# Kernel tuning notes

Hardware: AMD Instinct MI355X
Metric: run time of the kernel (lower is better)

## Reference

```python
import jax, jax.numpy as jnp
import numpy as np

B, S, E, H = 2, 2048, 1024, 16
Dh = E // H  # 64
KEEP = 0.9   # 1 - dropout_p
INV_SCALE = 1.0  # forward() default; call site does not pass inv_scale


def setup_inputs() -> dict:
    key = jax.random.key(0)
    ks = jax.random.split(key, 12)
    query = jax.random.normal(ks[0], (B, S, E), dtype=jnp.float32)
    key_t = jax.random.normal(ks[1], (B, S, E), dtype=jnp.float32)
    value = jax.random.normal(ks[2], (B, S, E), dtype=jnp.float32)
    attn_mask = jax.random.randint(ks[3], (B, S), 0, 2, dtype=jnp.int32)
    # pre-scaled inverted dropout keep-mask (deterministic stand-in for F.dropout)
    dropout_mask = (jax.random.uniform(ks[4], (B, H, S, S)) < KEEP).astype(jnp.float32) / KEEP
    Wq = jax.random.normal(ks[5], (E, E), dtype=jnp.float32) * 0.02
    bq = jnp.zeros((E,), dtype=jnp.float32)
    Wk = jax.random.normal(ks[6], (E, E), dtype=jnp.float32) * 0.02
    bk = jnp.zeros((E,), dtype=jnp.float32)
    Wv = jax.random.normal(ks[7], (E, E), dtype=jnp.float32) * 0.02
    bv = jnp.zeros((E,), dtype=jnp.float32)
    return {"query": query, "key": key_t, "value": value, "attn_mask": attn_mask,
            "dropout_mask": dropout_mask, "Wq": Wq, "bq": bq, "Wk": Wk, "bk": bk,
            "Wv": Wv, "bv": bv}


def _heads(x, W, b):
    # Linear then split heads: (B,S,E) -> (B,H,S,Dh)
    y = x @ W.T + b
    return y.reshape(B, S, H, Dh).transpose(0, 2, 1, 3)


def reference(query, key, value, attn_mask, dropout_mask, Wq, bq, Wk, bk, Wv, bv):
    q = _heads(query, Wq, bq)
    k = _heads(key, Wk, bk)
    v = _heads(value, Wv, bv)
    scores = jnp.einsum("bhqd,bhkd->bhqk", q, k) / INV_SCALE
    pad = (attn_mask == 0)[:, None, None, :]  # (B,1,1,S) True = masked
    scores = jnp.where(pad, -jnp.inf, scores)
    attn = jax.nn.softmax(scores, axis=-1) * dropout_mask
    out = jnp.einsum("bhqk,bhkd->bhqd", attn, v)  # (B,H,S,Dh)
    return out
```

## Files before the change

### kernel.cpp

```cpp
#include <hip/hip_runtime.h>

#define B_ 2
#define S_ 2048
#define E_ 1024
#define H_ 16
#define DH 64
#define MM (B_*S_)
#define BHN (B_*H_)

typedef unsigned short u16;
typedef unsigned int u32;
typedef __attribute__((ext_vector_type(8))) __bf16 bf16x8;
typedef __attribute__((ext_vector_type(4))) float f32x4;
typedef __attribute__((ext_vector_type(8))) u16 u16x8;
typedef __attribute__((ext_vector_type(4))) u16 u16x4;

static __device__ __forceinline__ u16 f2bf(float f) {
  u32 u = __builtin_bit_cast(u32, f);
  u += 0x7fffu + ((u >> 16) & 1u);
  return (u16)(u >> 16);
}
static __device__ __forceinline__ float bf2f(u16 h) {
  return __builtin_bit_cast(float, (u32)h << 16);
}
static __device__ __forceinline__ u32 sw(u32 byte) {
  return byte ^ (((byte >> 7) & 7u) << 4);
}
static __device__ __forceinline__ bf16x8 frag(const u16* lds, u32 byte) {
  return *(const bf16x8*)((const char*)lds + byte);
}
static __device__ __forceinline__ f32x4 mfma16(bf16x8 a, bf16x8 b, f32x4 c) {
  return __builtin_amdgcn_mfma_f32_16x16x32_bf16(a, b, c, 0, 0, 0);
}
static __device__ __forceinline__ void gload_lds16(const u16* g, u16* lds_base) {
  __builtin_amdgcn_global_load_lds(
      (const __attribute__((address_space(1))) u32*)g,
      (__attribute__((address_space(3))) u32*)lds_base, 16, 0, 0);
}

#define L2E 1.44269504088896340736f

struct SplitArg { const float* s; u16* h; u16* l; int n4; };

__global__ void split6_kernel(SplitArg a0, SplitArg a1, SplitArg a2,
                              SplitArg a3, SplitArg a4, SplitArg a5) {
  SplitArg A = (blockIdx.z == 0) ? a0 : (blockIdx.z == 1) ? a1 : (blockIdx.z == 2) ? a2
             : (blockIdx.z == 3) ? a3 : (blockIdx.z == 4) ? a4 : a5;
  int i = blockIdx.x * blockDim.x + threadIdx.x;
  int stride = gridDim.x * blockDim.x;
  if (A.l) {
    for (; i < A.n4; i += stride) {
      float4 v = ((const float4*)A.s)[i];
      u16x4 h, l;
      h.x = f2bf(v.x); l.x = f2bf(v.x - bf2f(h.x));
      h.y = f2bf(v.y); l.y = f2bf(v.y - bf2f(h.y));
      h.z = f2bf(v.z); l.z = f2bf(v.z - bf2f(h.z));
      h.w = f2bf(v.w); l.w = f2bf(v.w - bf2f(h.w));
      ((u16x4*)A.h)[i] = h;
      ((u16x4*)A.l)[i] = l;
    }
  } else {
    for (; i < A.n4; i += stride) {
      float4 v = ((const float4*)A.s)[i];
      u16x4 h;
      h.x = f2bf(v.x); h.y = f2bf(v.y); h.z = f2bf(v.z); h.w = f2bf(v.w);
      ((u16x4*)A.h)[i] = h;
    }
  }
}

__global__ void pack_mask(const int* __restrict__ am, u32* __restrict__ pm) {
  int w = threadIdx.x;
  if (w < 128) {
    int base = (w >> 6) * 2048 + (w & 63) * 32;
    u32 bits = 0;
#pragma unroll
    for (int j = 0; j < 8; ++j) {
      int4 v = *(const int4*)(am + base + j * 4);
      bits |= (v.x ? 1u : 0u) << (4 * j) | (v.y ? 1u : 0u) << (4 * j + 1) |
              (v.z ? 1u : 0u) << (4 * j + 2) | (v.w ? 1u : 0u) << (4 * j + 3);
    }
    pm[w] = bits;
  }
}

struct ProjArgs {
  const u16* xhi; const u16* xlo; const u16* whi; const u16* wlo;
  const float* bias; u16* ohi; u16* olo; int mode;
};

__global__ __launch_bounds__(256, 3) void proj_gemm(ProjArgs a0, ProjArgs a1, ProjArgs a2) {
  ProjArgs A = (blockIdx.z == 0) ? a0 : (blockIdx.z == 1) ? a1 : a2;
  __shared__ u16 As[128 * 64];
  __shared__ u16 Bs[128 * 64];
  const int t = threadIdx.x;
  const int l = t & 63, wid = t >> 6;
  const int g = l >> 4, ln = l & 15;
  const int wm = wid >> 1, wn = wid & 1;
  int bid = blockIdx.y * 8 + blockIdx.x;
  int sid = (bid & 7) * 32 + (bid >> 3);
  const int m0 = (sid >> 3) * 128, e0 = (sid & 7) * 128;

  f32x4 acc[4][4] = {};
  const int nkt = (A.mode == 2) ? 32 : 48;

  for (int kt = 0; kt < nkt; ++kt) {
    int kp = kt * 64;
    const u16* asrc = (kp < 2048) ? A.xhi : A.xlo;
    const u16* bsrc = (kp < 1024 || kp >= 2048) ? A.whi : A.wlo;
    int kc = kp & 1023;
#pragma unroll
    for (int r = 0; r < 4; ++r) {
      int cr = wid * 4 + r;
      int row = cr * 8 + (l >> 3);
      int col = (l & 7) * 8;
      gload_lds16(asrc + (size_t)(m0 + row) * 1024 + kc + col, As + cr * 512);
      gload_lds16(bsrc + (size_t)(e0 + row) * 1024 + kc + col, Bs + cr * 512);
    }
    __syncthreads();
#pragma unroll
    for (int ks = 0; ks < 2; ++ks) {
      bf16x8 af[4], bfv[4];
#pragma unroll
      for (int i = 0; i < 4; ++i) {
        af[i] = frag(As, (u32)(wm * 64 + i * 16 + ln) * 128 + ks * 64 + g * 16);
        bfv[i] = frag(Bs, (u32)(wn * 64 + i * 16 + ln) * 128 + ks * 64 + g * 16);
      }
#pragma unroll
      for (int i = 0; i < 4; ++i)
#pragma unroll
        for (int j = 0; j < 4; ++j)
          acc[i][j] = mfma16(af[i], bfv[j], acc[i][j]);
    }
    __syncthreads();
  }

#pragma unroll
  for (int i = 0; i < 4; ++i) {
#pragma unroll
    for (int j = 0; j < 4; ++j) {
      int e = e0 + wn * 64 + j * 16 + ln;
      int h = e >> 6, d = e & 63;
      float bias = A.bias[e];
      if (A.mode < 2) {
#pragma unroll
        for (int r = 0; r < 4; ++r) {
          int m = m0 + wm * 64 + i * 16 + g * 4 + r;
          float v = acc[i][j][r] + bias;
          if (A.mode == 0) v *= L2E;
          int b = m >> 11, s = m & 2047;
          size_t idx = ((size_t)((b * 16 + h) * 2048 + s)) * 64 + d;
          u16 hv = f2bf(v);
          A.ohi[idx] = hv;
          A.olo[idx] = f2bf(v - bf2f(hv));
        }
      } else {
        int m = m0 + wm * 64 + i * 16 + g * 4;
        int b = m >> 11, s = m & 2047;
        u16x4 pv;
#pragma unroll
        for (int r = 0; r < 4; ++r) pv[r] = f2bf(acc[i][j][r] + bias);
        size_t idx = ((size_t)((b * 16 + h) * 64 + d)) * 2048 + s;
        *(u16x4*)(A.ohi + idx) = pv;
      }
    }
  }
}

__global__ __launch_bounds__(256, 2) void attn_kernel(
    const u16* __restrict__ qhi, const u16* __restrict__ qlo,
    const u16* __restrict__ khi, const u16* __restrict__ klo,
    const u16* __restrict__ vt, const u32* __restrict__ pm,
    const float* __restrict__ dmask, float* __restrict__ out) {
  __shared__ u16 Ksh[2][64 * 64];
  __shared__ u16 Ksl[2][64 * 64];
  __shared__ u16 Vs[2][64 * 64];
  __shared__ u16 Ps[4 * 16 * 64];

  const int t = threadIdx.x, l = t & 63, wid = t >> 6;
  const int g = l >> 4, ln = l & 15;

  int bid = blockIdx.y * 32 + blockIdx.x;
  int sid = (bid & 7) * 128 + (bid >> 3);
  const int qt = sid & 31, bh = sid >> 5, b = bh >> 4;
  const int q0 = qt * 64;
  const int qrow = q0 + wid * 16 + ln;
  const size_t qg = ((size_t)bh * 2048 + qrow) * 64;
  const u32* pmb = pm + b * 64;

  bf16x8 qh[2], ql[2];
#pragma unroll
  for (int ks = 0; ks < 2; ++ks) {
    qh[ks] = *(const bf16x8*)(qhi + qg + ks * 32 + g * 8);
    ql[ks] = *(const bf16x8*)(qlo + qg + ks * 32 + g * 8);
  }

  const size_t dmrow = ((size_t)bh * 2048 + qrow) * 2048;
  float4 dmc[4], dmn[4];
  auto load_dm = [&](int kt, float4* d) {
    const int k0 = kt * 64;
#pragma unroll
    for (int i = 0; i < 4; ++i)
      d[i] = *(const float4*)(dmask + dmrow + k0 + i * 16 + 4 * g);
  };

  auto stage = [&](int buf, int kt) {
    const int k0 = kt * 64;
    const size_t kbase = ((size_t)bh * 2048 + k0) * 64;
    u16* khd = Ksh[buf];
    u16* kld = Ksl[buf];
    u16* vd = Vs[buf];
#pragma unroll
    for (int r = 0; r < 2; ++r) {
      int cbase = wid * 64 + 256 * r;
      int c = cbase + l;
      int c2 = c ^ ((c >> 3) & 7);
      gload_lds16(khi + kbase + c2 * 8, khd + cbase * 8);
      gload_lds16(klo + kbase + c2 * 8, kld + cbase * 8);
      gload_lds16(vt + ((size_t)bh * 64 + (c2 >> 3)) * 2048 + k0 + (c2 & 7) * 8,
                  vd + cbase * 8);
    }
  };

  load_dm(0, dmc);
  stage(0, 0);
  __syncthreads();

  f32x4 O[4] = {};
  float Zacc = 0.f;
  const u32 psbase = (u32)(wid * 2048 + ln * 128);

#pragma unroll 2
  for (int kt = 0; kt < 32; ++kt) {
    const int buf = kt & 1;
    if (kt < 31) {
      stage(buf ^ 1, kt + 1);
      load_dm(kt + 1, dmn);
    }
    u32 m0 = pmb[2 * kt], m1 = pmb[2 * kt + 1];

    f32x4 sc[4] = {};
#pragma unroll
    for (int ks = 0; ks < 2; ++ks) {
#pragma unroll
      for (int i = 0; i < 4; ++i) {
        u32 byt = sw((u32)((i * 16 + ln) * 128 + ks * 64 + g * 16));
        bf16x8 akh = frag(Ksh[buf], byt);
        bf16x8 akl = frag(Ksl[buf], byt);
        sc[i] = mfma16(akh, qh[ks], sc[i]);
        sc[i] = mfma16(akh, ql[ks], sc[i]);
        sc[i] = mfma16(akl, qh[ks], sc[i]);
      }
    }

#pragma unroll
    for (int i = 0; i < 4; ++i) {
      u32 mm = (i < 2 ? m0 : m1) >> (((i & 1) << 4) + 4 * g);
      float e0 = (mm & 1u) ? exp2f(sc[i][0]) : 0.f;
      float e1 = (mm & 2u) ? exp2f(sc[i][1]) : 0.f;
      float e2 = (mm & 4u) ? exp2f(sc[i][2]) : 0.f;
      float e3 = (mm & 8u) ? exp2f(sc[i][3]) : 0.f;
      Zacc += (e0 + e1) + (e2 + e3);
      u16x4 p;
      p.x = f2bf(e0 * dmc[i].x);
      p.y = f2bf(e1 * dmc[i].y);
      p.z = f2bf(e2 * dmc[i].z);
      p.w = f2bf(e3 * dmc[i].w);
      *(u16x4*)((char*)Ps + sw(psbase + i * 32 + g * 8)) = p;
    }

#pragma unroll
    for (int ks = 0; ks < 2; ++ks) {
      bf16x8 bP = frag(Ps, sw(psbase + ks * 64 + g * 16));
#pragma unroll
      for (int id = 0; id < 4; ++id) {
        bf16x8 aV = frag(Vs[buf], sw((u32)((id * 16 + ln) * 128 + ks * 64 + g * 16)));
        O[id] = mfma16(aV, bP, O[id]);
      }
    }

    __syncthreads();
    if (kt < 31) {
#pragma unroll
      for (int i = 0; i < 4; ++i) dmc[i] = dmn[i];
    }
  }

  float z = Zacc;
  z += __shfl_xor(z, 16, 64);
  z += __shfl_xor(z, 32, 64);
  float rz = 1.f / z;

#pragma unroll
  for (int id = 0; id < 4; ++id) {
    float4 o;
    o.x = O[id][0] * rz; o.y = O[id][1] * rz;
    o.z = O[id][2] * rz; o.w = O[id][3] * rz;
    *(float4*)(out + qg + id * 16 + 4 * g) = o;
  }
}

extern "C" void kernel_launch(void* const* d_in, const int* in_sizes, int n_in,
                              void* d_out, int out_size, void* d_ws, size_t ws_size,
                              hipStream_t stream) {
  const float* query = (const float*)d_in[0];
  const float* keyt  = (const float*)d_in[1];
  const float* value = (const float*)d_in[2];
  const int*   amask = (const int*)d_in[3];
  const float* dmask = (const float*)d_in[4];
  const float* Wq = (const float*)d_in[5];
  const float* bq = (const float*)d_in[6];
  const float* Wk = (const float*)d_in[7];
  const float* bk = (const float*)d_in[8];
  const float* Wv = (const float*)d_in[9];
  const float* bv = (const float*)d_in[10];

  char* ws = (char*)d_ws;
  size_t off = 0;
  auto alloc = [&](size_t bytes) {
    char* p = ws + off;
    off += (bytes + 255) & ~(size_t)255;
    return p;
  };
  const size_t XB = (size_t)MM * E_ * sizeof(u16);
  const size_t WB = (size_t)E_ * E_ * sizeof(u16);

  u16 *xh[3], *xl[3], *wh[3], *wl[3];
  for (int i = 0; i < 3; ++i) { xh[i] = (u16*)alloc(XB); xl[i] = (u16*)alloc(XB); }
  for (int i = 0; i < 3; ++i) { wh[i] = (u16*)alloc(WB); wl[i] = (u16*)alloc(WB); }
  u16* q_hi = (u16*)alloc(XB);
  u16* q_lo = (u16*)alloc(XB);
  u16* k_hi = (u16*)alloc(XB);
  u16* k_lo = (u16*)alloc(XB);
  u16* v_t  = (u16*)alloc(XB);
  u32* pmask = (u32*)alloc(512);
  if (off > ws_size) return;

  SplitArg sa[6] = {
      {query, xh[0], xl[0], MM * E_ / 4}, {keyt, xh[1], xl[1], MM * E_ / 4},
      {value, xh[2], nullptr, MM * E_ / 4}, {Wq, wh[0], wl[0], E_ * E_ / 4},
      {Wk, wh[1], wl[1], E_ * E_ / 4},    {Wv, wh[2], wl[2], E_ * E_ / 4},
  };
  split6_kernel<<<dim3(512, 1, 6), 256, 0, stream>>>(sa[0], sa[1], sa[2], sa[3], sa[4], sa[5]);
  pack_mask<<<1, 128, 0, stream>>>(amask, pmask);

  ProjArgs pa[3] = {
      {xh[0], xl[0], wh[0], wl[0], bq, q_hi, q_lo, 0},
      {xh[1], xl[1], wh[1], wl[1], bk, k_hi, k_lo, 1},
      {xh[2], nullptr, wh[2], wl[2], bv, v_t, nullptr, 2},
  };
  proj_gemm<<<dim3(8, 32, 3), 256, 0, stream>>>(pa[0], pa[1], pa[2]);

  attn_kernel<<<dim3(32, 32), 256, 0, stream>>>(
      q_hi, q_lo, k_hi, k_lo, v_t, pmask, dmask, (float*)d_out);
}
```

Measured before the change: 287.2 us.

## Process 128 query rows per attention block to reuse K/V tiles across two sub-tiles

Each wave now handles two 16-row query sub-tiles, so a block covers 128 query rows and the grid shrinks to 512 blocks. Every K/V tile staged in shared memory is reused for twice as many MFMAs, halving K/V global traffic per output. The dropout-mask prefetch into registers one iteration ahead is replaced by in-loop loads, and the unroll pragma is dropped. This raises register pressure and leaves fewer blocks to fill the CUs, and the dropout-mask stream, which dominates memory traffic, is unchanged.

New measurement: 327.5 us. +14.0%, slower.

```diff
diff --git a/kernel.cpp b/kernel.cpp
--- a/kernel.cpp
+++ b/kernel.cpp
@@ -175,34 +175,33 @@
   __shared__ u16 Ksh[2][64 * 64];
   __shared__ u16 Ksl[2][64 * 64];
   __shared__ u16 Vs[2][64 * 64];
-  __shared__ u16 Ps[4 * 16 * 64];
+  __shared__ u16 Ps[4 * 32 * 64];
 
   const int t = threadIdx.x, l = t & 63, wid = t >> 6;
   const int g = l >> 4, ln = l & 15;
 
-  int bid = blockIdx.y * 32 + blockIdx.x;
-  int sid = (bid & 7) * 128 + (bid >> 3);
-  const int qt = sid & 31, bh = sid >> 5, b = bh >> 4;
-  const int q0 = qt * 64;
-  const int qrow = q0 + wid * 16 + ln;
-  const size_t qg = ((size_t)bh * 2048 + qrow) * 64;
+  int bid = blockIdx.x;
+  int sid = (bid & 7) * 64 + (bid >> 3);
+  const int qt = sid & 15, bh = sid >> 4, b = bh >> 4;
+  const int q0 = qt * 128;
   const u32* pmb = pm + b * 64;
 
-  bf16x8 qh[2], ql[2];
-#pragma unroll
-  for (int ks = 0; ks < 2; ++ks) {
-    qh[ks] = *(const bf16x8*)(qhi + qg + ks * 32 + g * 8);
-    ql[ks] = *(const bf16x8*)(qlo + qg + ks * 32 + g * 8);
-  }
-
-  const size_t dmrow = ((size_t)bh * 2048 + qrow) * 2048;
-  float4 dmc[4], dmn[4];
-  auto load_dm = [&](int kt, float4* d) {
-    const int k0 = kt * 64;
-#pragma unroll
-    for (int i = 0; i < 4; ++i)
-      d[i] = *(const float4*)(dmask + dmrow + k0 + i * 16 + 4 * g);
-  };
+  size_t qg[2]; size_t dmrow[2];
+#pragma unroll
+  for (int qs = 0; qs < 2; ++qs) {
+    int qrow = q0 + wid * 32 + qs * 16 + ln;
+    qg[qs] = ((size_t)bh * 2048 + qrow) * 64;
+    dmrow[qs] = ((size_t)bh * 2048 + qrow) * 2048;
+  }
+
+  bf16x8 qh[2][2], ql[2][2];
+#pragma unroll
+  for (int qs = 0; qs < 2; ++qs)
+#pragma unroll
+    for (int ks = 0; ks < 2; ++ks) {
+      qh[qs][ks] = *(const bf16x8*)(qhi + qg[qs] + ks * 32 + g * 8);
+      ql[qs][ks] = *(const bf16x8*)(qlo + qg[qs] + ks * 32 + g * 8);
+    }
 
   auto stage = [&](int buf, int kt) {
     const int k0 = kt * 64;
@@ -222,24 +221,26 @@
     }
   };
 
-  load_dm(0, dmc);
   stage(0, 0);
   __syncthreads();
 
-  f32x4 O[4] = {};
-  float Zacc = 0.f;
-  const u32 psbase = (u32)(wid * 2048 + ln * 128);
-
-#pragma unroll 2
+  f32x4 O[2][4] = {};
+  float Zacc[2] = {0.f, 0.f};
+  const u32 psb = (u32)(wid * 4096);
+
   for (int kt = 0; kt < 32; ++kt) {
     const int buf = kt & 1;
-    if (kt < 31) {
-      stage(buf ^ 1, kt + 1);
-      load_dm(kt + 1, dmn);
-    }
+    const int k0 = kt * 64;
+    if (kt < 31) stage(buf ^ 1, kt + 1);
+    float4 dm[2][4];
+#pragma unroll
+    for (int qs = 0; qs < 2; ++qs)
+#pragma unroll
+      for (int i = 0; i < 4; ++i)
+        dm[qs][i] = *(const float4*)(dmask + dmrow[qs] + k0 + i * 16 + 4 * g);
     u32 m0 = pmb[2 * kt], m1 = pmb[2 * kt + 1];
 
-    f32x4 sc[4] = {};
+    f32x4 sc[2][4] = {};
 #pragma unroll
     for (int ks = 0; ks < 2; ++ks) {
 #pragma unroll
@@ -247,56 +248,61 @@
         u32 byt = sw((u32)((i * 16 + ln) * 128 + ks * 64 + g * 16));
         bf16x8 akh = frag(Ksh[buf], byt);
         bf16x8 akl = frag(Ksl[buf], byt);
-        sc[i] = mfma16(akh, qh[ks], sc[i]);
-        sc[i] = mfma16(akh, ql[ks], sc[i]);
-        sc[i] = mfma16(akl, qh[ks], sc[i]);
-      }
-    }
-
-#pragma unroll
-    for (int i = 0; i < 4; ++i) {
-      u32 mm = (i < 2 ? m0 : m1) >> (((i & 1) << 4) + 4 * g);
-      float e0 = (mm & 1u) ? exp2f(sc[i][0]) : 0.f;
-      float e1 = (mm & 2u) ? exp2f(sc[i][1]) : 0.f;
-      float e2 = (mm & 4u) ? exp2f(sc[i][2]) : 0.f;
-      float e3 = (mm & 8u) ? exp2f(sc[i][3]) : 0.f;
-      Zacc += (e0 + e1) + (e2 + e3);
-      u16x4 p;
-      p.x = f2bf(e0 * dmc[i].x);
-      p.y = f2bf(e1 * dmc[i].y);
-      p.z = f2bf(e2 * dmc[i].z);
-      p.w = f2bf(e3 * dmc[i].w);
-      *(u16x4*)((char*)Ps + sw(psbase + i * 32 + g * 8)) = p;
-    }
+#pragma unroll
+        for (int qs = 0; qs < 2; ++qs) {
+          sc[qs][i] = mfma16(akh, qh[qs][ks], sc[qs][i]);
+          sc[qs][i] = mfma16(akh, ql[qs][ks], sc[qs][i]);
+          sc[qs][i] = mfma16(akl, qh[qs][ks], sc[qs][i]);
+        }
+      }
+    }
+
+#pragma unroll
+    for (int qs = 0; qs < 2; ++qs)
+#pragma unroll
+      for (int i = 0; i < 4; ++i) {
+        u32 mm = (i < 2 ? m0 : m1) >> (((i & 1) << 4) + 4 * g);
+        float e0 = (mm & 1u) ? exp2f(sc[qs][i][0]) : 0.f;
+        float e1 = (mm & 2u) ? exp2f(sc[qs][i][1]) : 0.f;
+        float e2 = (mm & 4u) ? exp2f(sc[qs][i][2]) : 0.f;
+        float e3 = (mm & 8u) ? exp2f(sc[qs][i][3]) : 0.f;
+        Zacc[qs] += (e0 + e1) + (e2 + e3);
+        u16x4 p;
+        p.x = f2bf(e0 * dm[qs][i].x);
+        p.y = f2bf(e1 * dm[qs][i].y);
+        p.z = f2bf(e2 * dm[qs][i].z);
+        p.w = f2bf(e3 * dm[qs][i].w);
+        *(u16x4*)((char*)Ps + sw(psb + (qs * 16 + ln) * 128 + i * 32 + g * 8)) = p;
+      }
 
 #pragma unroll
     for (int ks = 0; ks < 2; ++ks) {
-      bf16x8 bP = frag(Ps, sw(psbase + ks * 64 + g * 16));
+      bf16x8 bP0 = frag(Ps, sw(psb + ln * 128 + ks * 64 + g * 16));
+      bf16x8 bP1 = frag(Ps, sw(psb + (16 + ln) * 128 + ks * 64 + g * 16));
 #pragma unroll
       for (int id = 0; id < 4; ++id) {
         bf16x8 aV = frag(Vs[buf], sw((u32)((id * 16 + ln) * 128 + ks * 64 + g * 16)));
-        O[id] = mfma16(aV, bP, O[id]);
+        O[0][id] = mfma16(aV, bP0, O[0][id]);
+        O[1][id] = mfma16(aV, bP1, O[1][id]);
       }
     }
 
     __syncthreads();
-    if (kt < 31) {
-#pragma unroll
-      for (int i = 0; i < 4; ++i) dmc[i] = dmn[i];
-    }
-  }
-
-  float z = Zacc;
-  z += __shfl_xor(z, 16, 64);
-  z += __shfl_xor(z, 32, 64);
-  float rz = 1.f / z;
-
-#pragma unroll
-  for (int id = 0; id < 4; ++id) {
-    float4 o;
-    o.x = O[id][0] * rz; o.y = O[id][1] * rz;
-    o.z = O[id][2] * rz; o.w = O[id][3] * rz;
-    *(float4*)(out + qg + id * 16 + 4 * g) = o;
+  }
+
+#pragma unroll
+  for (int qs = 0; qs < 2; ++qs) {
+    float z = Zacc[qs];
+    z += __shfl_xor(z, 16, 64);
+    z += __shfl_xor(z, 32, 64);
+    float rz = 1.f / z;
+#pragma unroll
+    for (int id = 0; id < 4; ++id) {
+      float4 o;
+      o.x = O[qs][id][0] * rz; o.y = O[qs][id][1] * rz;
+      o.z = O[qs][id][2] * rz; o.w = O[qs][id][3] * rz;
+      *(float4*)(out + qg[qs] + id * 16 + 4 * g) = o;
+    }
   }
 }
 
@@ -351,6 +357,6 @@
   };
   proj_gemm<<<dim3(8, 32, 3), 256, 0, stream>>>(pa[0], pa[1], pa[2]);
 
-  attn_kernel<<<dim3(32, 32), 256, 0, stream>>>(
+  attn_kernel<<<dim3(512), 256, 0, stream>>>(
       q_hi, q_lo, k_hi, k_lo, v_t, pmask, dmask, (float*)d_out);
 }
```
